# Performance work log

Measured on AMD Instinct MI355X. Metric: run time of the kernel, lower is better.

The kernel has to match this reference:

```python
import jax, jax.numpy as jnp
import numpy as np

N, E = 50000, 800000
IN_DIM, DIM, MP_STEPS, POS_DIM = 64, 128, 3, 3
EPS = 1e-5


def _ln(v):
    # LayerNorm without affine params (elementwise_affine=False)
    m = jnp.mean(v, axis=-1, keepdims=True)
    var = jnp.mean((v - m) ** 2, axis=-1, keepdims=True)
    return (v - m) * jax.lax.rsqrt(var + EPS)


def setup_inputs() -> dict:
    key = jax.random.key(0)
    ks = jax.random.split(key, 10)
    x = jax.random.normal(ks[0], (N, IN_DIM), dtype=jnp.float32)
    pos = jax.random.normal(ks[1], (N, POS_DIM), dtype=jnp.float32)
    edge_index = jax.random.randint(ks[2], (2, E), 0, N, dtype=jnp.int64)
    # Linear embed: torch Linear stores [out,in]; we store transposed [in,out]
    s_e = 1.0 / np.sqrt(IN_DIM)
    embed_w = jax.random.uniform(ks[3], (IN_DIM, DIM), jnp.float32, -s_e, s_e)
    embed_b = jax.random.uniform(ks[4], (DIM,), jnp.float32, -s_e, s_e)
    s_m = 1.0 / np.sqrt(2 * DIM + POS_DIM)
    msg_w = jax.random.uniform(ks[5], (MP_STEPS, 2 * DIM + POS_DIM, DIM), jnp.float32, -s_m, s_m)
    msg_b = jax.random.uniform(ks[6], (MP_STEPS, DIM), jnp.float32, -s_m, s_m)
    s_u = 1.0 / np.sqrt(2 * DIM)
    upd_w = jax.random.uniform(ks[7], (MP_STEPS, 2 * DIM, DIM), jnp.float32, -s_u, s_u)
    upd_b = jax.random.uniform(ks[8], (MP_STEPS, DIM), jnp.float32, -s_u, s_u)
    return {"x": x, "pos": pos, "edge_index": edge_index,
            "embed_w": embed_w, "embed_b": embed_b,
            "msg_w": msg_w, "msg_b": msg_b,
            "upd_w": upd_w, "upd_b": upd_b}


def reference(x, pos, edge_index, embed_w, embed_b, msg_w, msg_b, upd_w, upd_b):
    row, col = edge_index[0], edge_index[1]
    h = x @ embed_w + embed_b  # [N, DIM]
    # edge_attr computed under torch.no_grad -> constant
    edge_attr = jax.lax.stop_gradient(pos[row] - pos[col])  # [E, POS_DIM]
    ones = jnp.ones((E,), dtype=h.dtype)
    counts = jax.ops.segment_sum(ones, col, num_segments=N)  # [N]
    denom = jnp.maximum(counts, 1.0)[:, None]
    for s in range(MP_STEPS):
        mi = jnp.concatenate([h[row], h[col], edge_attr], axis=-1)  # [E, 2D+3]
        messages = _ln(jax.nn.gelu(mi @ msg_w[s] + msg_b[s], approximate=False))
        agg = jax.ops.segment_sum(messages, col, num_segments=N) / denom  # scatter_mean
        ui = jnp.concatenate([h, agg], axis=-1)  # [N, 2D]
        h = h + _ln(ui @ upd_w[s] + upd_b[s])
    return h
```

## Files before the change

### kernel.cpp

```cpp
#include <hip/hip_runtime.h>
#include <hip/hip_bf16.h>

#define NN 50000
#define NE 800000
#define IND 64
#define DIM 128
#define KUPD 256
#define NB_SCAN 196
#define NTILE 3125

typedef __attribute__((ext_vector_type(8))) short bf16x8;
typedef __attribute__((ext_vector_type(4))) short bf16x4;
typedef __attribute__((ext_vector_type(4))) float f32x4;
typedef __attribute__((ext_vector_type(2))) float f32x2;

static __device__ __forceinline__ short f2bf(float f) {
  union { __hip_bfloat16 b; short s; } u;
  u.b = __float2bfloat16(f);
  return u.s;
}
static __device__ __forceinline__ float bf2f(unsigned short u) {
  union { float f; unsigned int i; } x; x.i = ((unsigned int)u) << 16; return x.f;
}
static __device__ __forceinline__ float fexp2(float x) {
  float r; asm("v_exp_f32 %0, %1" : "=v"(r) : "v"(x)); return r;
}
static __device__ __forceinline__ float frcp(float x) {
  float r; asm("v_rcp_f32 %0, %1" : "=v"(r) : "v"(x)); return r;
}
static __device__ __forceinline__ float qsum16(float x) {
  x += __int_as_float(__builtin_amdgcn_mov_dpp(__float_as_int(x), 0x128, 0xf, 0xf, false));
  x += __int_as_float(__builtin_amdgcn_mov_dpp(__float_as_int(x), 0x124, 0xf, 0xf, false));
  x += __int_as_float(__builtin_amdgcn_mov_dpp(__float_as_int(x), 0x122, 0xf, 0xf, false));
  x += __int_as_float(__builtin_amdgcn_mov_dpp(__float_as_int(x), 0x121, 0xf, 0xf, false));
  return x;
}

__global__ __launch_bounds__(256) void embed_kernel(
    const float* __restrict__ x, const float* __restrict__ w,
    const float* __restrict__ b, short* __restrict__ hb) {
  __shared__ float ws[IND * DIM];
  __shared__ float xs[8 * IND];
  const int t = threadIdx.x;
  for (int i = t * 4; i < IND * DIM; i += 1024)
    *(float4*)(ws + i) = *(const float4*)(w + i);
  {
    int i = t * 4;
    if (i < 8 * IND)
      *(float4*)(xs + i) = *(const float4*)(x + (size_t)blockIdx.x * (8 * IND) + i);
  }
  __syncthreads();
  const int d = t & 127, g = t >> 7;
  const float bd = b[d];
  for (int nnod = g; nnod < 8; nnod += 2) {
    float acc = bd;
#pragma unroll
    for (int k = 0; k < IND; ++k) acc += xs[nnod * IND + k] * ws[k * DIM + d];
    const size_t n = (size_t)blockIdx.x * 8 + nnod;
    hb[n * DIM + d] = f2bf(acc);
  }
}

__global__ __launch_bounds__(256) void counts_kernel(const int* __restrict__ ei,
                                                     int* __restrict__ cnt) {
  int e = blockIdx.x * 256 + threadIdx.x;
  if (e < NE) atomicAdd(&cnt[ei[NE + e]], 1);
}

__global__ __launch_bounds__(256) void bsum_dhist_kernel(const int* __restrict__ cnt,
                                                         int* __restrict__ bsum,
                                                         int* __restrict__ dhist) {
  __shared__ int lh[64];
  __shared__ int wsum[4];
  int t = threadIdx.x, idx = blockIdx.x * 256 + t;
  if (t < 64) lh[t] = 0;
  __syncthreads();
  int c = (idx < NN) ? cnt[idx] : 0;
  int s = c;
#pragma unroll
  for (int m = 1; m < 64; m <<= 1) s += __shfl_xor(s, m, 64);
  if ((t & 63) == 0) wsum[t >> 6] = s;
  if (idx < NN) {
    int d = c > 63 ? 63 : c;
    atomicAdd(&lh[63 - d], 1);
  }
  __syncthreads();
  if (t == 0) bsum[blockIdx.x] = wsum[0] + wsum[1] + wsum[2] + wsum[3];
  if (t < 64 && lh[t] > 0) atomicAdd(&dhist[t], lh[t]);
}

__global__ __launch_bounds__(256) void bscan_dscan_kernel(const int* __restrict__ bsum,
                                                          int* __restrict__ boff,
                                                          const int* __restrict__ dhist,
                                                          int* __restrict__ dcur) {
  __shared__ int sh[256];
  int t = threadIdx.x;
  int v = (t < NB_SCAN) ? bsum[t] : 0;
  sh[t] = v;
  __syncthreads();
  for (int d = 1; d < 256; d <<= 1) {
    int u = (t >= d) ? sh[t - d] : 0;
    __syncthreads();
    sh[t] += u;
    __syncthreads();
  }
  if (t < NB_SCAN) boff[t] = sh[t] - v;
  if (t < 64) {
    int dv = dhist[t];
    int ds = dv;
    for (int d = 1; d < 64; d <<= 1) {
      int u = __shfl_up(ds, d, 64);
      if (t >= d) ds += u;
    }
    dcur[t] = ds - dv;
  }
}

__global__ __launch_bounds__(256) void final_scan_kernel(
    const int* __restrict__ cnt, const int* __restrict__ boff,
    int* __restrict__ dcur, const float* __restrict__ pos,
    int* __restrict__ off, int* __restrict__ cursor, float* __restrict__ rden,
    int* __restrict__ nodeOrd, float4* __restrict__ pos4g) {
  __shared__ int sh[256];
  __shared__ int lh[64];
  __shared__ int lbase[64];
  int b = blockIdx.x, t = threadIdx.x;
  int idx = b * 256 + t;
  bool act = (idx < NN);
  int c = act ? cnt[idx] : 0;
  if (t < 64) lh[t] = 0;
  sh[t] = c;
  __syncthreads();
  for (int d = 1; d < 256; d <<= 1) {
    int u = (t >= d) ? sh[t - d] : 0;
    __syncthreads();
    sh[t] += u;
    __syncthreads();
  }
  int bin = 63 - (c > 63 ? 63 : c);
  int lrank = 0;
  if (act) {
    int e = boff[b] + sh[t] - c;
    off[idx] = e;
    cursor[idx] = e;
    rden[idx] = 1.0f / fmaxf((float)c, 1.0f);
    pos4g[idx] = make_float4(pos[3 * idx], pos[3 * idx + 1], pos[3 * idx + 2], 0.f);
    lrank = atomicAdd(&lh[bin], 1);
  }
  __syncthreads();
  if (t < 64) lbase[t] = (lh[t] > 0) ? atomicAdd(&dcur[t], lh[t]) : 0;
  __syncthreads();
  if (act) nodeOrd[lbase[bin] + lrank] = idx;
  if (b == 0 && t == 0) off[NN] = NE;
}

__global__ __launch_bounds__(256) void scatter_kernel(const int* __restrict__ ei,
                                                      int* __restrict__ cursor,
                                                      int* __restrict__ rowOf) {
  int e = blockIdx.x * 256 + threadIdx.x;
  if (e < NE) {
    int c = ei[NE + e];
    int p = atomicAdd(&cursor[c], 1);
    rowOf[p] = ei[e];
  }
}

__global__ __launch_bounds__(256) void wt_all_kernel(const float* __restrict__ wm,
                                                     const float* __restrict__ wu,
                                                     short* __restrict__ wt12,
                                                     short* __restrict__ wtu) {
  int i = blockIdx.x * 256 + threadIdx.x;
  if (i < 3 * 256 * DIM) {
    int k = i % DIM, o = (i / DIM) % 256, s = i / (DIM * 256);
    int krow = (o < DIM) ? k : (DIM + k);
    int d = o & (DIM - 1);
    wt12[i] = f2bf(wm[((size_t)s * 259 + krow) * DIM + d]);
  } else {
    int j = i - 3 * 256 * DIM;
    if (j < 3 * DIM * KUPD) {
      int k = j % KUPD, d = (j / KUPD) % DIM, s = j / (KUPD * DIM);
      wtu[j] = f2bf(wu[((size_t)s * KUPD + k) * DIM + d]);
    }
  }
}

__global__ __launch_bounds__(512) void p12_kernel(const short* __restrict__ hb,
                                                  const short* __restrict__ wt12_s,
                                                  short* __restrict__ P12b) {
  __shared__ short wlds[256][136];
  const int t = threadIdx.x;
  const int wid = t >> 6, lane = t & 63;
  const int m = lane & 15, kg = lane >> 4;
  for (int i = t * 8; i < 256 * DIM; i += 512 * 8) {
    int r = i >> 7, c = i & 127;
    *(bf16x8*)(&wlds[r][c]) = *(const bf16x8*)(wt12_s + i);
  }
  __syncthreads();
  const int wgid = blockIdx.x * 8 + wid;
#pragma unroll
  for (int rep = 0; rep < 2; ++rep) {
    int tid = wgid + rep * 2048;
    if (tid >= NTILE) break;
    int nbase = tid * 16;
    const short* hrow = hb + (size_t)(nbase + m) * DIM;
    bf16x8 bfrag[4];
#pragma unroll
    for (int cc = 0; cc < 4; ++cc)
      bfrag[cc] = *(const bf16x8*)(hrow + cc * 32 + kg * 8);
#pragma unroll
    for (int half = 0; half < 2; ++half) {
      f32x4 acc[8];
#pragma unroll
      for (int i = 0; i < 8; ++i) acc[i] = (f32x4)0.0f;
#pragma unroll
      for (int cc = 0; cc < 4; ++cc) {
#pragma unroll
        for (int tl = 0; tl < 8; ++tl) {
          bf16x8 afrag = *(const bf16x8*)(&wlds[half * DIM + tl * 16 + m][cc * 32 + kg * 8]);
          acc[tl] = __builtin_amdgcn_mfma_f32_16x16x32_bf16(afrag, bfrag[cc], acc[tl], 0, 0, 0);
        }
      }
#pragma unroll
      for (int tl = 0; tl < 8; ++tl) {
        bf16x4 p;
#pragma unroll
        for (int j = 0; j < 4; ++j) p[j] = f2bf(acc[tl][j]);
        *(bf16x4*)(P12b + (size_t)(nbase + m) * 256 + half * DIM + tl * 16 + kg * 4) = p;
      }
    }
  }
}

__global__ __launch_bounds__(256) void msg_agg_kernel(
    const short* __restrict__ P12b, const float4* __restrict__ pos4g,
    const int* __restrict__ rowOf, const int* __restrict__ off,
    const int* __restrict__ nodeOrd, const float* __restrict__ rden,
    const float* __restrict__ wmsg_s,
    const float* __restrict__ bias_s, short* __restrict__ aggb) {
  const int t = threadIdx.x;
  const int wid = t >> 6, lane = t & 63;
  const int n = nodeOrd[blockIdx.x * 4 + wid];
  const int q = lane >> 4;
  const int d0 = (lane & 15) * 8;
  f32x2 w30v[4], w31v[4], w32v[4], pbv[4];
  {
    const float* w30p = wmsg_s + 256 * DIM + d0;
    const float* w31p = wmsg_s + 257 * DIM + d0;
    const float* w32p = wmsg_s + 258 * DIM + d0;
    bf16x8 p2v = *(const bf16x8*)(P12b + (size_t)n * 256 + DIM + d0);
#pragma unroll
    for (int p = 0; p < 4; ++p) {
      w30v[p] = *(const f32x2*)(w30p + 2 * p);
      w31v[p] = *(const f32x2*)(w31p + 2 * p);
      w32v[p] = *(const f32x2*)(w32p + 2 * p);
      f32x2 bb = *(const f32x2*)(bias_s + d0 + 2 * p);
      pbv[p].x = bf2f((unsigned short)p2v[2 * p]) + bb.x;
      pbv[p].y = bf2f((unsigned short)p2v[2 * p + 1]) + bb.y;
    }
  }
  const float4 pc = pos4g[n];
  const int start = off[n], end = off[n + 1];
  f32x2 av[4];
#pragma unroll
  for (int p = 0; p < 4; ++p) av[p] = (f32x2)0.0f;
  float bacc = 0.f;
  const f32x2 gc1 = (f32x2)(-0.102951604f);
  const f32x2 gc0 = (f32x2)(-2.30234934f);
  const f32x2 onev = (f32x2)1.0f;
  if (start < end) {
    const int last = end - 1;
    int ia = start + q; if (ia > last) ia = last;
    int ra = rowOf[ia];
    bf16x8 p1a = *(const bf16x8*)(P12b + (size_t)ra * 256 + d0);
    float4 ppa = pos4g[ra];
    int ib = start + 4 + q; if (ib > last) ib = last;
    int rb = rowOf[ib];
    bf16x8 p1b = *(const bf16x8*)(P12b + (size_t)rb * 256 + d0);
    float4 ppb = pos4g[rb];
#pragma unroll 2
    for (int jg = start; jg < end; jg += 4) {
      int ic = jg + 8 + q; if (ic > last) ic = last;
      int rc = rowOf[ic];
      bf16x8 p1c = *(const bf16x8*)(P12b + (size_t)rc * 256 + d0);
      float4 ppc = pos4g[rc];
      f32x2 e0v = (f32x2)(ppa.x - pc.x);
      f32x2 e1v = (f32x2)(ppa.y - pc.y);
      f32x2 e2v = (f32x2)(ppa.z - pc.z);
      f32x2 g[4];
      f32x2 s1v = (f32x2)0.0f, s2v = (f32x2)0.0f;
#pragma unroll
      for (int p = 0; p < 4; ++p) {
        unsigned int u = ((const unsigned int*)&p1a)[p];
        f32x2 v;
        v.x = __uint_as_float(u << 16);
        v.y = __uint_as_float(u & 0xffff0000u);
        v = v + pbv[p];
        v = __builtin_elementwise_fma(e2v, w32v[p], v);
        v = __builtin_elementwise_fma(e1v, w31v[p], v);
        v = __builtin_elementwise_fma(e0v, w30v[p], v);
        f32x2 u2 = v * v;
        f32x2 wv = __builtin_elementwise_fma(u2, gc1, gc0);
        f32x2 zv = v * wv;
        f32x2 tv;
        tv.x = fexp2(zv.x);
        tv.y = fexp2(zv.y);
        tv = tv + onev;
        f32x2 rv;
        rv.x = frcp(tv.x);
        rv.y = frcp(tv.y);
        f32x2 gg = v * rv;
        g[p] = gg;
        s1v = s1v + gg;
        s2v = __builtin_elementwise_fma(gg, gg, s2v);
      }
      float s1 = s1v.x + s1v.y;
      float s2 = s2v.x + s2v.y;
      s1 = qsum16(s1);
      s2 = qsum16(s2);
      float mean = s1 * (1.0f / 128.0f);
      float tvv = fmaf(mean, -mean, 1e-5f);
      float var = fmaf(s2, 1.0f / 128.0f, tvv);
      float rstd = rsqrtf(var);
      float rs = (jg + q < end) ? rstd : 0.0f;
      bacc = fmaf(mean, rs, bacc);
      f32x2 rsv = (f32x2)rs;
#pragma unroll
      for (int p = 0; p < 4; ++p) av[p] = __builtin_elementwise_fma(g[p], rsv, av[p]);
      p1a = p1b; ppa = ppb;
      p1b = p1c; ppb = ppc;
    }
  }
  const float rd = rden[n];
  float out[8];
#pragma unroll
  for (int p = 0; p < 4; ++p) {
    out[2 * p] = av[p].x - bacc;
    out[2 * p + 1] = av[p].y - bacc;
  }
  bf16x8 ob;
#pragma unroll
  for (int k = 0; k < 8; ++k) {
    out[k] += __shfl_xor(out[k], 16, 64);
    out[k] += __shfl_xor(out[k], 32, 64);
    ob[k] = f2bf(out[k] * rd);
  }
  if (q == 0)
    *(bf16x8*)(aggb + (size_t)n * DIM + d0) = ob;
}

template <int FINAL>
__global__ __launch_bounds__(512) void upd_kernel(
    const short* hb, const short* __restrict__ aggb,
    const short* __restrict__ wt,
    const float* __restrict__ bias, float* __restrict__ h, short* hbo) {
  __shared__ short wlds[DIM][264];
  const int t = threadIdx.x;
  const int wid = t >> 6, lane = t & 63;
  const int m = lane & 15, kg = lane >> 4;
  for (int i = t * 8; i < DIM * 256; i += 512 * 8) {
    int r = i >> 8, c = i & 255;
    *(bf16x8*)(&wlds[r][c]) = *(const bf16x8*)(wt + i);
  }
  __syncthreads();
  const int wgid = blockIdx.x * 8 + wid;
#pragma unroll
  for (int rep = 0; rep < 2; ++rep) {
    int tid = wgid + rep * 2048;
    if (tid >= NTILE) break;
    int nbase = tid * 16;
    const int nA = nbase + m;
    const short* hrow = hb + (size_t)nA * DIM;
    const short* arow = aggb + (size_t)nA * DIM;

    f32x4 acc[8];
#pragma unroll
    for (int i = 0; i < 8; ++i) acc[i] = (f32x4)0.0f;
#pragma unroll
    for (int cc = 0; cc < 8; ++cc) {
      bf16x8 a = (cc < 4) ? *(const bf16x8*)(hrow + cc * 32 + kg * 8)
                          : *(const bf16x8*)(arow + (cc - 4) * 32 + kg * 8);
#pragma unroll
      for (int tl = 0; tl < 8; ++tl) {
        bf16x8 bfr = *(const bf16x8*)(&wlds[tl * 16 + m][cc * 32 + kg * 8]);
        acc[tl] = __builtin_amdgcn_mfma_f32_16x16x32_bf16(a, bfr, acc[tl], 0, 0, 0);
      }
    }

    float s1[4] = {0.f, 0.f, 0.f, 0.f}, s2[4] = {0.f, 0.f, 0.f, 0.f};
#pragma unroll
    for (int tl = 0; tl < 8; ++tl) {
      float bd = bias[tl * 16 + m];
#pragma unroll
      for (int j = 0; j < 4; ++j) {
        float xv = acc[tl][j] + bd;
        acc[tl][j] = xv;
        s1[j] += xv;
        s2[j] = fmaf(xv, xv, s2[j]);
      }
    }
#pragma unroll
    for (int mask = 1; mask < 16; mask <<= 1) {
#pragma unroll
      for (int j = 0; j < 4; ++j) {
        s1[j] += __shfl_xor(s1[j], mask, 64);
        s2[j] += __shfl_xor(s2[j], mask, 64);
      }
    }
#pragma unroll
    for (int j = 0; j < 4; ++j) {
      float mean = s1[j] * (1.0f / 128.0f);
      float var = s2[j] * (1.0f / 128.0f) - mean * mean;
      float rstd = rsqrtf(var + 1e-5f);
      int nw = nbase + kg * 4 + j;
#pragma unroll
      for (int tl = 0; tl < 8; ++tl) {
        int d = tl * 16 + m;
        float res = bf2f((unsigned short)hb[(size_t)nw * DIM + d]);
        float hv = res + (acc[tl][j] - mean) * rstd;
        hbo[(size_t)nw * DIM + d] = f2bf(hv);
        if (FINAL) h[(size_t)nw * DIM + d] = hv;
      }
    }
  }
}

extern "C" void kernel_launch(void* const* d_in, const int* in_sizes, int n_in,
                              void* d_out, int out_size, void* d_ws, size_t ws_size,
                              hipStream_t stream) {
  const float* x       = (const float*)d_in[0];
  const float* pos     = (const float*)d_in[1];
  const int* ei        = (const int*)d_in[2];
  const float* embed_w = (const float*)d_in[3];
  const float* embed_b = (const float*)d_in[4];
  const float* msg_w   = (const float*)d_in[5];
  const float* msg_b   = (const float*)d_in[6];
  const float* upd_w   = (const float*)d_in[7];
  const float* upd_b   = (const float*)d_in[8];
  float* h = (float*)d_out;

  char* ws = (char*)d_ws;
  size_t off_b = 0;
  short* hb     = (short*)(ws + off_b);  off_b += (size_t)NN * DIM * 2;
  short* P12b   = (short*)(ws + off_b);  off_b += (size_t)NN * 256 * 2;
  short* aggb   = (short*)(ws + off_b);  off_b += (size_t)NN * DIM * 2;
  float* rden   = (float*)(ws + off_b);  off_b += (size_t)NN * 4;
  int*   cnt    = (int*)(ws + off_b);    off_b += (size_t)NN * 4;
  int*   offs   = (int*)(ws + off_b);    off_b += (size_t)(NN + 16) * 4;
  int*   cursor = (int*)(ws + off_b);    off_b += (size_t)NN * 4;
  int*   rowOf  = (int*)(ws + off_b);    off_b += (size_t)NE * 4;
  int*   bsum   = (int*)(ws + off_b);    off_b += (size_t)256 * 4;
  int*   boff   = (int*)(ws + off_b);    off_b += (size_t)256 * 4;
  int*   dhist  = (int*)(ws + off_b);    off_b += (size_t)64 * 4;
  int*   dcur   = (int*)(ws + off_b);    off_b += (size_t)64 * 4;
  int*   nodeOrd= (int*)(ws + off_b);    off_b += (size_t)NN * 4;
  float4* pos4g = (float4*)(ws + off_b); off_b += (size_t)NN * 16;
  short* wt12   = (short*)(ws + off_b);  off_b += (size_t)3 * 256 * DIM * 2;
  short* wtu    = (short*)(ws + off_b);  off_b += (size_t)3 * DIM * KUPD * 2;

  hipMemsetAsync(cnt, 0, (size_t)NN * 4, stream);
  hipMemsetAsync(dhist, 0, 64 * 4, stream);
  counts_kernel<<<(NE + 255) / 256, 256, 0, stream>>>(ei, cnt);
  bsum_dhist_kernel<<<NB_SCAN, 256, 0, stream>>>(cnt, bsum, dhist);
  bscan_dscan_kernel<<<1, 256, 0, stream>>>(bsum, boff, dhist, dcur);
  final_scan_kernel<<<NB_SCAN, 256, 0, stream>>>(cnt, boff, dcur, pos,
                                                 offs, cursor, rden, nodeOrd, pos4g);
  scatter_kernel<<<(NE + 255) / 256, 256, 0, stream>>>(ei, cursor, rowOf);
  wt_all_kernel<<<(3 * 256 * DIM + 3 * DIM * KUPD + 255) / 256, 256, 0, stream>>>(
      msg_w, upd_w, wt12, wtu);
  embed_kernel<<<NN / 8, 256, 0, stream>>>(x, embed_w, embed_b, hb);

  for (int s = 0; s < 3; ++s) {
    p12_kernel<<<256, 512, 0, stream>>>(hb, wt12 + (size_t)s * 256 * DIM, P12b);
    msg_agg_kernel<<<NN / 4, 256, 0, stream>>>(P12b, pos4g, rowOf, offs, nodeOrd, rden,
                                               msg_w + (size_t)s * 259 * DIM,
                                               msg_b + (size_t)s * DIM, aggb);
    if (s < 2)
      upd_kernel<0><<<256, 512, 0, stream>>>(hb, aggb, wtu + (size_t)s * DIM * KUPD,
                                             upd_b + (size_t)s * DIM, h, hb);
    else
      upd_kernel<1><<<256, 512, 0, stream>>>(hb, aggb, wtu + (size_t)s * DIM * KUPD,
                                             upd_b + (size_t)s * DIM, h, hb);
  }
}
```

Before: 420.2 us.

## Fuse next-step P12 projection into update kernel; skip final bf16 h write

The update kernel now also computes the next step's node projections (P12) right after writing the updated h tile, reusing the same blocks and tile assignment. Each wave reads back its own freshly written h rows, which removes two separate p12 launches and their h reload from a cold cache. The final step skips the unused bf16 h write. Risks include the extra LDS weight reload, the larger shared array reducing occupancy, and reading hbo rows written by other lanes of the same wave without an explicit fence.

```diff
diff --git a/kernel.cpp b/kernel.cpp
--- a/kernel.cpp
+++ b/kernel.cpp
@@ -187,13 +187,13 @@
 __global__ __launch_bounds__(512) void p12_kernel(const short* __restrict__ hb,
                                                   const short* __restrict__ wt12_s,
                                                   short* __restrict__ P12b) {
-  __shared__ short wlds[256][136];
+  __shared__ short wlds[256 * 132];
   const int t = threadIdx.x;
   const int wid = t >> 6, lane = t & 63;
   const int m = lane & 15, kg = lane >> 4;
   for (int i = t * 8; i < 256 * DIM; i += 512 * 8) {
     int r = i >> 7, c = i & 127;
-    *(bf16x8*)(&wlds[r][c]) = *(const bf16x8*)(wt12_s + i);
+    *(bf16x8*)(&wlds[r * 132 + c]) = *(const bf16x8*)(wt12_s + i);
   }
   __syncthreads();
   const int wgid = blockIdx.x * 8 + wid;
@@ -216,7 +216,7 @@
       for (int cc = 0; cc < 4; ++cc) {
 #pragma unroll
         for (int tl = 0; tl < 8; ++tl) {
-          bf16x8 afrag = *(const bf16x8*)(&wlds[half * DIM + tl * 16 + m][cc * 32 + kg * 8]);
+          bf16x8 afrag = *(const bf16x8*)(&wlds[(half * DIM + tl * 16 + m) * 132 + cc * 32 + kg * 8]);
           acc[tl] = __builtin_amdgcn_mfma_f32_16x16x32_bf16(afrag, bfrag[cc], acc[tl], 0, 0, 0);
         }
       }
@@ -349,17 +349,19 @@
 }
 
 template <int FINAL>
-__global__ __launch_bounds__(512) void upd_kernel(
+__global__ __launch_bounds__(512) void updp12_kernel(
     const short* hb, const short* __restrict__ aggb,
-    const short* __restrict__ wt,
-    const float* __restrict__ bias, float* __restrict__ h, short* hbo) {
-  __shared__ short wlds[DIM][264];
+    const short* __restrict__ wtu_s,
+    const short* __restrict__ wt12_n,
+    const float* __restrict__ bias, float* __restrict__ h, short* hbo,
+    short* __restrict__ P12b) {
+  __shared__ short wlds[33792];
   const int t = threadIdx.x;
   const int wid = t >> 6, lane = t & 63;
   const int m = lane & 15, kg = lane >> 4;
   for (int i = t * 8; i < DIM * 256; i += 512 * 8) {
     int r = i >> 8, c = i & 255;
-    *(bf16x8*)(&wlds[r][c]) = *(const bf16x8*)(wt + i);
+    *(bf16x8*)(&wlds[r * 264 + c]) = *(const bf16x8*)(wtu_s + i);
   }
   __syncthreads();
   const int wgid = blockIdx.x * 8 + wid;
@@ -381,7 +383,7 @@
                           : *(const bf16x8*)(arow + (cc - 4) * 32 + kg * 8);
 #pragma unroll
       for (int tl = 0; tl < 8; ++tl) {
-        bf16x8 bfr = *(const bf16x8*)(&wlds[tl * 16 + m][cc * 32 + kg * 8]);
+        bf16x8 bfr = *(const bf16x8*)(&wlds[(tl * 16 + m) * 264 + cc * 32 + kg * 8]);
         acc[tl] = __builtin_amdgcn_mfma_f32_16x16x32_bf16(a, bfr, acc[tl], 0, 0, 0);
       }
     }
@@ -417,8 +419,48 @@
         int d = tl * 16 + m;
         float res = bf2f((unsigned short)hb[(size_t)nw * DIM + d]);
         float hv = res + (acc[tl][j] - mean) * rstd;
-        hbo[(size_t)nw * DIM + d] = f2bf(hv);
         if (FINAL) h[(size_t)nw * DIM + d] = hv;
+        else       hbo[(size_t)nw * DIM + d] = f2bf(hv);
+      }
+    }
+  }
+  if (FINAL) return;
+
+  __syncthreads();
+  for (int i = t * 8; i < 256 * DIM; i += 512 * 8) {
+    int r = i >> 7, c = i & 127;
+    *(bf16x8*)(&wlds[r * 132 + c]) = *(const bf16x8*)(wt12_n + i);
+  }
+  __syncthreads();
+#pragma unroll
+  for (int rep = 0; rep < 2; ++rep) {
+    int tid = wgid + rep * 2048;
+    if (tid >= NTILE) break;
+    int nbase = tid * 16;
+    const short* hrow = hbo + (size_t)(nbase + m) * DIM;
+    bf16x8 bfrag[4];
+#pragma unroll
+    for (int cc = 0; cc < 4; ++cc)
+      bfrag[cc] = *(const bf16x8*)(hrow + cc * 32 + kg * 8);
+#pragma unroll
+    for (int half = 0; half < 2; ++half) {
+      f32x4 acc[8];
+#pragma unroll
+      for (int i = 0; i < 8; ++i) acc[i] = (f32x4)0.0f;
+#pragma unroll
+      for (int cc = 0; cc < 4; ++cc) {
+#pragma unroll
+        for (int tl = 0; tl < 8; ++tl) {
+          bf16x8 afrag = *(const bf16x8*)(&wlds[(half * DIM + tl * 16 + m) * 132 + cc * 32 + kg * 8]);
+          acc[tl] = __builtin_amdgcn_mfma_f32_16x16x32_bf16(afrag, bfrag[cc], acc[tl], 0, 0, 0);
+        }
+      }
+#pragma unroll
+      for (int tl = 0; tl < 8; ++tl) {
+        bf16x4 p;
+#pragma unroll
+        for (int j = 0; j < 4; ++j) p[j] = f2bf(acc[tl][j]);
+        *(bf16x4*)(P12b + (size_t)(nbase + m) * 256 + half * DIM + tl * 16 + kg * 4) = p;
       }
     }
   }
@@ -447,7 +489,7 @@
   int*   cnt    = (int*)(ws + off_b);    off_b += (size_t)NN * 4;
   int*   offs   = (int*)(ws + off_b);    off_b += (size_t)(NN + 16) * 4;
   int*   cursor = (int*)(ws + off_b);    off_b += (size_t)NN * 4;
-  int*   rowOf  = (int*)(ws + off_b);    off_b += (size_t)NE * 4;
+  int*   rowOf  = (int*)(ws + off_b);    off_b += (size_t)(NE + 16) * 4;
   int*   bsum   = (int*)(ws + off_b);    off_b += (size_t)256 * 4;
   int*   boff   = (int*)(ws + off_b);    off_b += (size_t)256 * 4;
   int*   dhist  = (int*)(ws + off_b);    off_b += (size_t)64 * 4;
@@ -468,17 +510,21 @@
   wt_all_kernel<<<(3 * 256 * DIM + 3 * DIM * KUPD + 255) / 256, 256, 0, stream>>>(
       msg_w, upd_w, wt12, wtu);
   embed_kernel<<<NN / 8, 256, 0, stream>>>(x, embed_w, embed_b, hb);
+  p12_kernel<<<256, 512, 0, stream>>>(hb, wt12, P12b);
 
   for (int s = 0; s < 3; ++s) {
-    p12_kernel<<<256, 512, 0, stream>>>(hb, wt12 + (size_t)s * 256 * DIM, P12b);
     msg_agg_kernel<<<NN / 4, 256, 0, stream>>>(P12b, pos4g, rowOf, offs, nodeOrd, rden,
                                                msg_w + (size_t)s * 259 * DIM,
                                                msg_b + (size_t)s * DIM, aggb);
     if (s < 2)
-      upd_kernel<0><<<256, 512, 0, stream>>>(hb, aggb, wtu + (size_t)s * DIM * KUPD,
-                                             upd_b + (size_t)s * DIM, h, hb);
+      updp12_kernel<0><<<256, 512, 0, stream>>>(
+          hb, aggb, wtu + (size_t)s * DIM * KUPD,
+          wt12 + (size_t)(s + 1) * 256 * DIM,
+          upd_b + (size_t)s * DIM, h, hb, P12b);
     else
-      upd_kernel<1><<<256, 512, 0, stream>>>(hb, aggb, wtu + (size_t)s * DIM * KUPD,
-                                             upd_b + (size_t)s * DIM, h, hb);
-  }
-}
+      updp12_kernel<1><<<256, 512, 0, stream>>>(
+          hb, aggb, wtu + (size_t)s * DIM * KUPD,
+          wt12,
+          upd_b + (size_t)s * DIM, h, hb, P12b);
+  }
+}
```

Measured after the change: 413.0 us. Within noise of the previous version (-1.7%).
